# Optimization experiments

Measured on AMD Instinct MI355X. Metric: run time of the kernel, lower is better.

Reference implementation:

```python
import jax, jax.numpy as jnp
import numpy as np

B, M, L, D = 4, 128, 512, 768
NEG = -1e30


def setup_inputs() -> dict:
    key = jax.random.key(0)
    k1, k2 = jax.random.split(key)
    h = jax.random.normal(k1, (B, L, D), dtype=jnp.float32)
    mention_masks = jax.random.randint(k2, (B, M, L), 0, 2, dtype=jnp.int32)
    return {"h": h, "mention_masks": mention_masks}


def reference(h, mention_masks):
    # h: [B, L, D]; mention_masks: [B, M, L] (0/1)
    # Faithful to: m = (mask == 0).float() * -1e30; (m + h).max(dim=2)
    m = (mention_masks == 0).astype(h.dtype) * NEG          # [B, M, L]
    # broadcast add then max over token dim L -> [B, M, D]
    mention_reprs = jnp.max(h[:, None, :, :] + m[:, :, :, None], axis=2)
    return mention_reprs
```

## Files before the change

### kernel.cpp

```cpp
#include <hip/hip_runtime.h>

#define BB 4
#define MM 128
#define LL 512
#define DD 768
#define NEGF (-1e30f)

__global__ __launch_bounds__(1024, 4) void mention_max_kernel(
    const float* __restrict__ h, const int* __restrict__ mask,
    float* __restrict__ out)
{
    const int lane = threadIdx.x & 63;
    const int wave = threadIdx.x >> 6;

    const int flat  = blockIdx.x;
    const int slice = flat & 15;
    const int mch   = flat >> 4;
    const int b     = slice >> 2;
    const int dch   = slice & 3;

    const int m0 = mch * 8;
    const int l0 = wave * 32;

    const int half = lane >> 5;
    const int lrow = lane & 31;
    const int* mp = mask + ((size_t)(b * MM + m0)) * LL + l0 + lrow;
    const int mv0 = mp[(0 + half) * LL];
    const int mv1 = mp[(2 + half) * LL];
    const int mv2 = mp[(4 + half) * LL];
    const int mv3 = mp[(6 + half) * LL];

    unsigned wbits[8];
    { unsigned long long bl = __ballot(mv0 != 0);
      wbits[0] = __builtin_amdgcn_readfirstlane((unsigned)bl);
      wbits[1] = __builtin_amdgcn_readfirstlane((unsigned)(bl >> 32)); }
    { unsigned long long bl = __ballot(mv1 != 0);
      wbits[2] = __builtin_amdgcn_readfirstlane((unsigned)bl);
      wbits[3] = __builtin_amdgcn_readfirstlane((unsigned)(bl >> 32)); }
    { unsigned long long bl = __ballot(mv2 != 0);
      wbits[4] = __builtin_amdgcn_readfirstlane((unsigned)bl);
      wbits[5] = __builtin_amdgcn_readfirstlane((unsigned)(bl >> 32)); }
    { unsigned long long bl = __ballot(mv3 != 0);
      wbits[6] = __builtin_amdgcn_readfirstlane((unsigned)bl);
      wbits[7] = __builtin_amdgcn_readfirstlane((unsigned)(bl >> 32)); }

    __builtin_amdgcn_sched_barrier(0);

    const float* glane = h + ((size_t)(b * LL + l0)) * DD + dch * 192 + lane;

    float sx[12], sy[12], sz[12];

#define ISSUE_ROW(ROW, S) do {                                                \
        const float* _a = glane + (size_t)(ROW) * DD;                         \
        asm volatile("global_load_dword %0, %1, off"                          \
                     : "=v"(sx[S]) : "v"(_a) : "memory");                     \
        asm volatile("global_load_dword %0, %1, off offset:256"               \
                     : "=v"(sy[S]) : "v"(_a) : "memory");                     \
        asm volatile("global_load_dword %0, %1, off offset:512"               \
                     : "=v"(sz[S]) : "v"(_a) : "memory");                     \
    } while (0)

#define WAITROW_(N, S)                                                        \
    asm volatile("s_waitcnt vmcnt(" #N ")"                                    \
                 : "+v"(sx[S]), "+v"(sy[S]), "+v"(sz[S]) :: "memory")
#define WAITROW(N, S) WAITROW_(N, S)

    float accx[8], accy[8], accz[8];
#pragma unroll
    for (int m = 0; m < 8; ++m) { accx[m] = NEGF; accy[m] = NEGF; accz[m] = NEGF; }

#define CONSUME(I, S) do {                                                    \
        const float vx = sx[S], vy = sy[S], vz = sz[S];                       \
        _Pragma("unroll")                                                     \
        for (int m = 0; m < 8; ++m) {                                         \
            if ((wbits[m] >> (I)) & 1u) {                                     \
                accx[m] = fmaxf(accx[m], vx);                                 \
                accy[m] = fmaxf(accy[m], vy);                                 \
                accz[m] = fmaxf(accz[m], vz);                                 \
            }                                                                 \
        }                                                                     \
    } while (0)

    ISSUE_ROW(0, 0);  ISSUE_ROW(1, 1);  ISSUE_ROW(2, 2);  ISSUE_ROW(3, 3);
    ISSUE_ROW(4, 4);  ISSUE_ROW(5, 5);  ISSUE_ROW(6, 6);  ISSUE_ROW(7, 7);
    ISSUE_ROW(8, 8);  ISSUE_ROW(9, 9);  ISSUE_ROW(10, 10); ISSUE_ROW(11, 11);

#define STEP(I, S) do { WAITROW(33, S); CONSUME(I, S); ISSUE_ROW((I) + 12, S); } while (0)
    STEP(0, 0);   STEP(1, 1);   STEP(2, 2);   STEP(3, 3);
    STEP(4, 4);   STEP(5, 5);   STEP(6, 6);   STEP(7, 7);
    STEP(8, 8);   STEP(9, 9);   STEP(10, 10); STEP(11, 11);
    STEP(12, 0);  STEP(13, 1);  STEP(14, 2);  STEP(15, 3);
    STEP(16, 4);  STEP(17, 5);  STEP(18, 6);  STEP(19, 7);
#undef STEP

#define DSTEP(I, S, N) do { WAITROW(N, S); CONSUME(I, S); } while (0)
    DSTEP(20, 8, 33);  DSTEP(21, 9, 30);  DSTEP(22, 10, 27); DSTEP(23, 11, 24);
    DSTEP(24, 0, 21);  DSTEP(25, 1, 18);  DSTEP(26, 2, 15);  DSTEP(27, 3, 12);
    DSTEP(28, 4, 9);   DSTEP(29, 5, 6);   DSTEP(30, 6, 3);   DSTEP(31, 7, 0);
#undef DSTEP
#undef CONSUME
#undef WAITROW
#undef WAITROW_
#undef ISSUE_ROW

    __shared__ float red[8][8][3][64];
    if (wave >= 8) {
#pragma unroll
        for (int m = 0; m < 8; ++m) {
            red[wave - 8][m][0][lane] = accx[m];
            red[wave - 8][m][1][lane] = accy[m];
            red[wave - 8][m][2][lane] = accz[m];
        }
    }
    __syncthreads();
    if (wave < 8) {
#pragma unroll
        for (int m = 0; m < 8; ++m) {
            red[wave][m][0][lane] = fmaxf(accx[m], red[wave][m][0][lane]);
            red[wave][m][1][lane] = fmaxf(accy[m], red[wave][m][1][lane]);
            red[wave][m][2][lane] = fmaxf(accz[m], red[wave][m][2][lane]);
        }
    }
    __syncthreads();

    if (threadIdx.x < 512) {
        const int m  = (int)(threadIdx.x >> 6);
        const int ln = (int)(threadIdx.x & 63);
        float vx = red[0][m][0][ln];
        float vy = red[0][m][1][ln];
        float vz = red[0][m][2][ln];
#pragma unroll
        for (int w = 1; w < 8; ++w) {
            vx = fmaxf(vx, red[w][m][0][ln]);
            vy = fmaxf(vy, red[w][m][1][ln]);
            vz = fmaxf(vz, red[w][m][2][ln]);
        }
        float* op = out + ((size_t)(b * MM + m0 + m)) * DD + dch * 192;
        op[ln]       = vx;
        op[64 + ln]  = vy;
        op[128 + ln] = vz;
    }
}

extern "C" void kernel_launch(void* const* d_in, const int* in_sizes, int n_in,
                              void* d_out, int out_size, void* d_ws, size_t ws_size,
                              hipStream_t stream) {
    const float* h    = (const float*)d_in[0];
    const int*   mask = (const int*)d_in[1];
    float*       out  = (float*)d_out;
    mention_max_kernel<<<dim3(256), dim3(1024), 0, stream>>>(h, mask, out);
}
```

Baseline: 67.80 us.

## Split mention max into LDS-staged L-chunk partials plus workspace reduction

Adds a two-kernel path. The first kernel stages a 64-row by 192-column tile of h into LDS with global_load_lds, and all 64 mentions of one (batch, mention-half) group reuse that tile. It writes per-L-chunk partial maxima to the workspace, and a second kernel max-reduces the 8 partials into the output. This cuts the number of times h is re-read from memory, from once per 8 mentions to once per 64. The cost is about 12 MB of workspace writes and reads plus an extra launch, and the original single kernel remains as a fallback when the workspace is too small.

```diff
diff --git a/kernel.cpp b/kernel.cpp
--- a/kernel.cpp
+++ b/kernel.cpp
@@ -5,6 +5,144 @@
 #define LL 512
 #define DD 768
 #define NEGF (-1e30f)
+
+
+typedef __attribute__((address_space(1))) const unsigned int gu32_t;
+typedef __attribute__((address_space(3))) unsigned int lu32_t;
+
+#define PARTIAL_FLOATS (64 * 768)
+#define WS_FLOATS (64 * PARTIAL_FLOATS)
+#define LCH_STRIDE (8 * PARTIAL_FLOATS)
+
+__global__ __launch_bounds__(1024, 4) void mention_part_kernel(
+    const float* __restrict__ h, const int* __restrict__ mask,
+    float* __restrict__ ws)
+{
+    const int lane = threadIdx.x & 63;
+    const int wave = threadIdx.x >> 6;
+
+    const int flat = blockIdx.x;
+    const int grp  = flat & 7;
+    const int b    = grp >> 1;
+    const int mch  = grp & 1;
+    const int inner = flat >> 3;
+    const int dch  = inner >> 3;
+    const int lch  = inner & 7;
+
+    const int l0   = lch * 64;
+    const int mloc0 = wave * 4;
+
+    __shared__ float hs[64 * 192];
+
+    const int* mp = mask +
+        ((size_t)(b * MM + mch * 64 + mloc0)) * LL + l0 + lane;
+    const int mv0 = mp[0 * LL];
+    const int mv1 = mp[1 * LL];
+    const int mv2 = mp[2 * LL];
+    const int mv3 = mp[3 * LL];
+
+    const float* hrow = h + ((size_t)(b * LL + l0)) * DD + dch * 192;
+#define STAGE_ROW(R) do {                                                     \
+        const float* _s = hrow + (size_t)(R) * DD;                            \
+        float* _d = hs + (R) * 192;                                           \
+        __builtin_amdgcn_global_load_lds((gu32_t*)(_s + 0 * 64 + lane),       \
+                                         (lu32_t*)(_d + 0 * 64), 4, 0, 0);    \
+        __builtin_amdgcn_global_load_lds((gu32_t*)(_s + 1 * 64 + lane),       \
+                                         (lu32_t*)(_d + 1 * 64), 4, 0, 0);    \
+        __builtin_amdgcn_global_load_lds((gu32_t*)(_s + 2 * 64 + lane),       \
+                                         (lu32_t*)(_d + 2 * 64), 4, 0, 0);    \
+    } while (0)
+    STAGE_ROW(2 * wave);
+    STAGE_ROW(2 * wave + 1);
+
+    unsigned blo[4], bhi[4];
+    { unsigned long long bl = __ballot(mv0 != 0);
+      blo[0] = __builtin_amdgcn_readfirstlane((unsigned)bl);
+      bhi[0] = __builtin_amdgcn_readfirstlane((unsigned)(bl >> 32)); }
+    { unsigned long long bl = __ballot(mv1 != 0);
+      blo[1] = __builtin_amdgcn_readfirstlane((unsigned)bl);
+      bhi[1] = __builtin_amdgcn_readfirstlane((unsigned)(bl >> 32)); }
+    { unsigned long long bl = __ballot(mv2 != 0);
+      blo[2] = __builtin_amdgcn_readfirstlane((unsigned)bl);
+      bhi[2] = __builtin_amdgcn_readfirstlane((unsigned)(bl >> 32)); }
+    { unsigned long long bl = __ballot(mv3 != 0);
+      blo[3] = __builtin_amdgcn_readfirstlane((unsigned)bl);
+      bhi[3] = __builtin_amdgcn_readfirstlane((unsigned)(bl >> 32)); }
+
+    __syncthreads();
+
+    STAGE_ROW(32 + 2 * wave);
+    STAGE_ROW(33 + 2 * wave);
+#undef STAGE_ROW
+
+    float ax[4], ay[4], az[4];
+#pragma unroll
+    for (int q = 0; q < 4; ++q) { ax[q] = NEGF; ay[q] = NEGF; az[q] = NEGF; }
+
+#define CHALF(BASE, W)                                                        \
+    _Pragma("unroll")                                                         \
+    for (int r = 0; r < 32; r += 2) {                                         \
+        const float* rp0 = hs + (BASE + r) * 192;                             \
+        const float* rp1 = rp0 + 192;                                         \
+        const float x0 = rp0[lane], y0 = rp0[64 + lane], z0 = rp0[128 + lane];\
+        const float x1 = rp1[lane], y1 = rp1[64 + lane], z1 = rp1[128 + lane];\
+        _Pragma("unroll")                                                     \
+        for (int q = 0; q < 4; ++q) {                                         \
+            const float ad0 = ((W[q] >> r) & 1u) ? 0.0f : NEGF;               \
+            const float ad1 = ((W[q] >> (r + 1)) & 1u) ? 0.0f : NEGF;         \
+            ax[q] = fmaxf(fmaxf(x0 + ad0, x1 + ad1), ax[q]);                  \
+            ay[q] = fmaxf(fmaxf(y0 + ad0, y1 + ad1), ay[q]);                  \
+            az[q] = fmaxf(fmaxf(z0 + ad0, z1 + ad1), az[q]);                  \
+        }                                                                     \
+    }
+
+    CHALF(0, blo)
+    __syncthreads();
+    CHALF(32, bhi)
+#undef CHALF
+
+    float* wp = ws + ((size_t)(lch * 8 + grp)) * PARTIAL_FLOATS
+                   + (size_t)mloc0 * 768 + dch * 192;
+#pragma unroll
+    for (int q = 0; q < 4; ++q) {
+        wp[q * 768 + lane]       = ax[q];
+        wp[q * 768 + 64 + lane]  = ay[q];
+        wp[q * 768 + 128 + lane] = az[q];
+    }
+}
+
+__global__ __launch_bounds__(1024) void mention_reduce_kernel(
+    const float* __restrict__ ws, float* __restrict__ out)
+{
+    const int flat = blockIdx.x;
+    const int grp  = flat & 7;
+    const int j    = flat >> 3;
+    const int b    = grp >> 1;
+    const int mch  = grp & 1;
+    const int mloc = j * 2;
+
+#pragma unroll
+    for (int e0 = 0; e0 < 2; ++e0) {
+        const int e = (int)threadIdx.x + e0 * 1024;
+        if (e < 1536) {
+            const int m_ = e >> 9 >= 0 ? (e / 768) : 0;
+            const int d  = e - m_ * 768;
+            const float* p = ws + (size_t)grp * PARTIAL_FLOATS
+                                + (size_t)(mloc + m_) * 768 + d;
+            const float v0 = p[(size_t)0 * LCH_STRIDE];
+            const float v1 = p[(size_t)1 * LCH_STRIDE];
+            const float v2 = p[(size_t)2 * LCH_STRIDE];
+            const float v3 = p[(size_t)3 * LCH_STRIDE];
+            const float v4 = p[(size_t)4 * LCH_STRIDE];
+            const float v5 = p[(size_t)5 * LCH_STRIDE];
+            const float v6 = p[(size_t)6 * LCH_STRIDE];
+            const float v7 = p[(size_t)7 * LCH_STRIDE];
+            const float v = fmaxf(fmaxf(fmaxf(v0, v1), fmaxf(v2, v3)),
+                                  fmaxf(fmaxf(v4, v5), fmaxf(v6, v7)));
+            out[((size_t)(b * MM + mch * 64 + mloc + m_)) * DD + d] = v;
+        }
+    }
+}
 
 __global__ __launch_bounds__(1024, 4) void mention_max_kernel(
     const float* __restrict__ h, const int* __restrict__ mask,
@@ -47,7 +185,6 @@
     __builtin_amdgcn_sched_barrier(0);
 
     const float* glane = h + ((size_t)(b * LL + l0)) * DD + dch * 192 + lane;
-
     float sx[12], sy[12], sz[12];
 
 #define ISSUE_ROW(ROW, S) do {                                                \
@@ -59,7 +196,6 @@
         asm volatile("global_load_dword %0, %1, off offset:512"               \
                      : "=v"(sz[S]) : "v"(_a) : "memory");                     \
     } while (0)
-
 #define WAITROW_(N, S)                                                        \
     asm volatile("s_waitcnt vmcnt(" #N ")"                                    \
                  : "+v"(sx[S]), "+v"(sy[S]), "+v"(sz[S]) :: "memory")
@@ -92,7 +228,6 @@
     STEP(12, 0);  STEP(13, 1);  STEP(14, 2);  STEP(15, 3);
     STEP(16, 4);  STEP(17, 5);  STEP(18, 6);  STEP(19, 7);
 #undef STEP
-
 #define DSTEP(I, S, N) do { WAITROW(N, S); CONSUME(I, S); } while (0)
     DSTEP(20, 8, 33);  DSTEP(21, 9, 30);  DSTEP(22, 10, 27); DSTEP(23, 11, 24);
     DSTEP(24, 0, 21);  DSTEP(25, 1, 18);  DSTEP(26, 2, 15);  DSTEP(27, 3, 12);
@@ -148,5 +283,11 @@
     const float* h    = (const float*)d_in[0];
     const int*   mask = (const int*)d_in[1];
     float*       out  = (float*)d_out;
-    mention_max_kernel<<<dim3(256), dim3(1024), 0, stream>>>(h, mask, out);
-}
+    if (d_ws != nullptr && ws_size >= (size_t)WS_FLOATS * sizeof(float)) {
+        float* ws = (float*)d_ws;
+        mention_part_kernel<<<dim3(256), dim3(1024), 0, stream>>>(h, mask, ws);
+        mention_reduce_kernel<<<dim3(256), dim3(1024), 0, stream>>>(ws, out);
+    } else {
+        mention_max_kernel<<<dim3(256), dim3(1024), 0, stream>>>(h, mask, out);
+    }
+}
```

Result: slower. 72.75 us (+7.3%).
